# Kernel tuning notes

Measured on AMD Instinct MI355X. Metric: run time of the kernel, lower is better.

## Reference

```python
import jax, jax.numpy as jnp
import numpy as np

B, S, H, V = 4, 512, 256, 32000


def setup_inputs() -> dict:
    key = jax.random.key(0)
    ks = jax.random.split(key, 6)
    s = 0.02
    x = jax.random.randint(ks[0], (B, S), 0, V)
    emb = jax.random.normal(ks[1], (V, H), dtype=jnp.float32) * s
    W_ih = jax.random.normal(ks[2], (3 * H, H), dtype=jnp.float32) * s
    W_hh = jax.random.normal(ks[3], (3 * H, H), dtype=jnp.float32) * s
    b_ih = jnp.zeros((3 * H,), jnp.float32)
    b_hh = jnp.zeros((3 * H,), jnp.float32)
    W_out = jax.random.normal(ks[4], (V, H), dtype=jnp.float32) * s
    b_out = jnp.zeros((V,), jnp.float32)
    return dict(x=x, emb=emb, W_ih=W_ih, W_hh=W_hh, b_ih=b_ih, b_hh=b_hh,
                W_out=W_out, b_out=b_out)


def gru_sequence(embedded, W_ih, W_hh, b_ih, b_hh):
    # embedded: [B, S, H]; precompute all input projections once: [B, S, 3H]
    xp = jnp.einsum('bsh,gh->bsg', embedded, W_ih) + b_ih
    Hdim = W_hh.shape[1]
    h0 = jnp.zeros((embedded.shape[0], Hdim), embedded.dtype)

    def step(h, xt):  # xt: [B, 3H]
        hp = h @ W_hh.T + b_hh  # [B, 3H]
        xr, xz, xn = jnp.split(xt, 3, axis=-1)
        hr, hz, hn = jnp.split(hp, 3, axis=-1)
        r = jax.nn.sigmoid(xr + hr)
        z = jax.nn.sigmoid(xz + hz)
        n = jnp.tanh(xn + r * hn)
        h_new = (1.0 - z) * n + z * h
        return h_new, h_new

    _, hs = jax.lax.scan(step, h0, jnp.swapaxes(xp, 0, 1))  # [S, B, H]
    return jnp.swapaxes(hs, 0, 1)  # [B, S, H]


def reference(x, emb, W_ih, W_hh, b_ih, b_hh, W_out, b_out):
    embedded = emb[x]                                   # [B, S, H]
    rnn_out = gru_sequence(embedded, W_ih, W_hh, b_ih, b_hh)
    logits = jnp.einsum('bsh,vh->bsv', rnn_out, W_out) + b_out  # [B, S, V]
    # symbolic constraint: if prev token == 0, tokens >= 3 are invalid (t > 0)
    prev_zero = (x[:, :-1] == 0)                        # [B, S-1]
    prev_zero = jnp.pad(prev_zero, ((0, 0), (1, 0)))    # t=0 never masked
    vocab_ge3 = jnp.arange(logits.shape[-1]) >= 3       # [V]
    invalid = prev_zero[:, :, None] & vocab_ge3[None, None, :]
    return jnp.where(invalid, -jnp.inf, logits)
```

## Files before the change

### kernel.cpp

```cpp
#include <hip/hip_runtime.h>
#include <hip/hip_bf16.h>

typedef __attribute__((ext_vector_type(8))) short bf16x8;
typedef __attribute__((ext_vector_type(4))) float f32x4;
typedef __attribute__((ext_vector_type(4))) unsigned short u16x4;

#define HB 256
#define G3 768
#define SQ 512
#define NBATCH 4
#define NV 32000

__device__ __forceinline__ unsigned short f2bf(float f) {
    unsigned int u = __float_as_uint(f);
    u = u + 0x7FFFu + ((u >> 16) & 1u);
    return (unsigned short)(u >> 16);
}

__global__ void k_prep(const float* __restrict__ W_ih, const float* __restrict__ W_hh,
                       const float* __restrict__ W_out, float* __restrict__ w_ihT,
                       unsigned short* __restrict__ wfrag, unsigned short* __restrict__ woutbf,
                       int do_wout) {
    int stride = gridDim.x * blockDim.x;
    int tid = blockIdx.x * blockDim.x + threadIdx.x;
    for (int e = tid; e < G3 * HB; e += stride) {
        int k = e / G3, g = e - k * G3;
        w_ihT[e] = W_ih[g * HB + k];
    }
    for (int e = tid; e < G3 * HB; e += stride) {
        int i = e & 7, l = (e >> 3) & 63, c = (e >> 9) & 7, s = (e >> 12) & 3;
        int q = e >> 14;
        int g = q % 3, w = q / 3;
        int row = g * 256 + 64 * w + 16 * s + (l & 15);
        int kk = 32 * c + 8 * (l >> 4) + i;
        wfrag[e] = f2bf(W_hh[row * HB + kk]);
    }
    if (do_wout) {
        for (int e = tid; e < NV * HB; e += stride) woutbf[e] = f2bf(W_out[e]);
    }
}

__global__ __launch_bounds__(256) void k_embed_xp(
        const int* __restrict__ x, const float* __restrict__ emb,
        const float* __restrict__ w_ihT, const float* __restrict__ b_ih,
        const float* __restrict__ b_hh, float* __restrict__ xp) {
    __shared__ float e[8][HB];
    int tid = threadIdx.x;
    int tok0 = blockIdx.x * 8;
    {
        int s = tid >> 5, k0 = (tid & 31) * 8;
        long idx = x[tok0 + s];
        const float* src = emb + idx * (long)HB + k0;
        f32x4 a = *(const f32x4*)src, bq = *(const f32x4*)(src + 4);
        *(f32x4*)&e[s][k0] = a;
        *(f32x4*)&e[s][k0 + 4] = bq;
    }
    __syncthreads();
    #pragma unroll
    for (int it = 0; it < 3; ++it) {
        int gg = tid + it * 256;
        float acc[8] = {0.f, 0.f, 0.f, 0.f, 0.f, 0.f, 0.f, 0.f};
        for (int k = 0; k < HB; k += 4) {
            float w0 = w_ihT[(k + 0) * G3 + gg];
            float w1 = w_ihT[(k + 1) * G3 + gg];
            float w2 = w_ihT[(k + 2) * G3 + gg];
            float w3 = w_ihT[(k + 3) * G3 + gg];
            #pragma unroll
            for (int s = 0; s < 8; ++s) {
                f32x4 ev = *(const f32x4*)&e[s][k];
                acc[s] += w0 * ev.x + w1 * ev.y + w2 * ev.z + w3 * ev.w;
            }
        }
        float bias = b_ih[gg] + (gg < 512 ? b_hh[gg] : 0.f);
        #pragma unroll
        for (int s = 0; s < 8; ++s)
            xp[(size_t)(tok0 + s) * G3 + gg] = acc[s] + bias;
    }
}

__global__ __attribute__((amdgpu_waves_per_eu(1, 1))) __launch_bounds__(256)
void k_gru(const float* __restrict__ xp, const unsigned short* __restrict__ wfrag,
           const float* __restrict__ b_hh, unsigned short* __restrict__ rnn) {
    __shared__ unsigned short hbf[2][NBATCH][HB];

    int tid = threadIdx.x;
    int w = tid >> 6, l = tid & 63;
    int c15 = l & 15, hi = l >> 4;
    int b4 = c15 & 3;
    int g4 = c15 >> 2;
    int swz = (b4 & 1) << 6;

    bf16x8 Arz[2][4][8];
    bf16x8 An[4][8];
    #pragma unroll
    for (int g = 0; g < 2; ++g)
        #pragma unroll
        for (int s = 0; s < 4; ++s)
            #pragma unroll
            for (int c = 0; c < 8; ++c) {
                Arz[g][s][c] = ((const bf16x8*)wfrag)[(((w * 3 + g) * 4 + s) * 8 + c) * 64 + l];
                asm volatile("" : "+a"(Arz[g][s][c]));
            }
    #pragma unroll
    for (int s = 0; s < 4; ++s)
        #pragma unroll
        for (int c = 0; c < 8; ++c) {
            An[s][c] = ((const bf16x8*)wfrag)[(((w * 3 + 2) * 4 + c) * 8 + 0) * 64 + l];
            An[s][c] = ((const bf16x8*)wfrag)[(((w * 3 + 2) * 4 + s) * 8 + c) * 64 + l];
            asm volatile("" : "+v"(An[s][c]));
        }

    for (int k = tid; k < 2 * NBATCH * HB; k += 256) ((unsigned short*)hbf)[k] = 0;

    int iL = 64 * w + 16 * g4 + 4 * hi;
    f32x4 bnv = *(const f32x4*)&b_hh[512 + iL];
    f32x4 H = {0.f, 0.f, 0.f, 0.f};
    const f32x4 zz = {0.f, 0.f, 0.f, 0.f};

    const float* xpb = xp + (size_t)b4 * SQ * G3 + iL;
    unsigned short* rnb = rnn + (size_t)b4 * SQ * HB + iL;
    __syncthreads();

    for (int t = 0; t < SQ; ++t) {
        int cur = t & 1, nxt = cur ^ 1;
        const char* hbb = (const char*)hbf + cur * 2048 + b4 * 512;

        f32x4 xr = *(const f32x4*)(xpb);
        f32x4 xz = *(const f32x4*)(xpb + 256);
        f32x4 xn = *(const f32x4*)(xpb + 512);

        f32x4 ar[4], az[4], an[4];
        #pragma unroll
        for (int s = 0; s < 4; ++s) { ar[s] = zz; az[s] = zz; an[s] = zz; }

        #pragma unroll
        for (int c = 0; c < 8; ++c) {
            bf16x8 Bf = *(const bf16x8*)(hbb + ((64 * c + 16 * hi) ^ swz));
            #pragma unroll
            for (int s = 0; s < 4; ++s) {
                asm("v_mfma_f32_16x16x32_bf16 %0, %1, %2, %0"
                    : "+v"(ar[s]) : "a"(Arz[0][s][c]), "v"(Bf));
                asm("v_mfma_f32_16x16x32_bf16 %0, %1, %2, %0"
                    : "+v"(az[s]) : "a"(Arz[1][s][c]), "v"(Bf));
                an[s] = __builtin_amdgcn_mfma_f32_16x16x32_bf16(An[s][c], Bf, an[s], 0, 0, 0);
            }
        }
        asm volatile("s_nop 7\n\ts_nop 7"
                     : "+v"(ar[0]), "+v"(ar[1]), "+v"(ar[2]), "+v"(ar[3]),
                       "+v"(az[0]), "+v"(az[1]), "+v"(az[2]), "+v"(az[3]));

        bool s1 = (g4 & 1) != 0, s2 = (g4 & 2) != 0;
        f32x4 sAr = s2 ? (s1 ? ar[3] : ar[2]) : (s1 ? ar[1] : ar[0]);
        f32x4 sAz = s2 ? (s1 ? az[3] : az[2]) : (s1 ? az[1] : az[0]);
        f32x4 sAn = s2 ? (s1 ? an[3] : an[2]) : (s1 ? an[1] : an[0]);

        u16x4 pack;
        #pragma unroll
        for (int j = 0; j < 4; ++j) {
            float r = __builtin_amdgcn_rcpf(1.f + __expf(-(xr[j] + sAr[j])));
            float z = __builtin_amdgcn_rcpf(1.f + __expf(-(xz[j] + sAz[j])));
            float narg = xn[j] + r * (sAn[j] + bnv[j]);
            float n = 1.f - 2.f * __builtin_amdgcn_rcpf(__expf(2.f * narg) + 1.f);
            float hv = (1.f - z) * n + z * H[j];
            H[j] = hv;
            pack[j] = f2bf(hv);
        }
        *(u16x4*)((char*)hbf + nxt * 2048 + b4 * 512 + ((iL * 2) ^ swz)) = pack;
        *(u16x4*)rnb = pack;

        __syncthreads();
        xpb += G3;
        rnb += HB;
    }
}

template <int CONV>
__global__ __launch_bounds__(256) void k_logits(
        const unsigned short* __restrict__ rnn, const unsigned short* __restrict__ woutbf,
        const float* __restrict__ woutf, const float* __restrict__ b_out,
        const int* __restrict__ x, float* __restrict__ out) {
    int tid = threadIdx.x;
    int wv = tid >> 6, l = tid & 63;
    int wm = wv >> 1, wn = wv & 1;
    int c15 = l & 15, hi = l >> 4;
    int m0 = blockIdx.y * 128 + wm * 64;
    int n0 = blockIdx.x * 128 + wn * 64;

    const f32x4 zz = {0.f, 0.f, 0.f, 0.f};
    f32x4 acc[4][4];
    #pragma unroll
    for (int i = 0; i < 4; ++i)
        #pragma unroll
        for (int j = 0; j < 4; ++j) acc[i][j] = zz;

    #pragma unroll
    for (int c = 0; c < 8; ++c) {
        bf16x8 af[4], bfr[4];
        #pragma unroll
        for (int rt = 0; rt < 4; ++rt)
            af[rt] = *(const bf16x8*)(rnn + (size_t)(m0 + rt * 16 + c15) * HB + 32 * c + 8 * hi);
        #pragma unroll
        for (int ct = 0; ct < 4; ++ct) {
            if (CONV) {
                const float* s = woutf + (size_t)(n0 + ct * 16 + c15) * HB + 32 * c + 8 * hi;
                f32x4 lo = *(const f32x4*)s, hi4 = *(const f32x4*)(s + 4);
                bf16x8 bb;
                #pragma unroll
                for (int q = 0; q < 4; ++q) bb[q] = (short)f2bf(lo[q]);
                #pragma unroll
                for (int q = 0; q < 4; ++q) bb[4 + q] = (short)f2bf(hi4[q]);
                bfr[ct] = bb;
            } else {
                bfr[ct] = *(const bf16x8*)(woutbf + (size_t)(n0 + ct * 16 + c15) * HB + 32 * c + 8 * hi);
            }
        }
        #pragma unroll
        for (int rt = 0; rt < 4; ++rt)
            #pragma unroll
            for (int ct = 0; ct < 4; ++ct)
                acc[rt][ct] = __builtin_amdgcn_mfma_f32_16x16x32_bf16(af[rt], bfr[ct], acc[rt][ct], 0, 0, 0);
    }

    float bo[4];
    #pragma unroll
    for (int ct = 0; ct < 4; ++ct) bo[ct] = b_out[n0 + ct * 16 + c15];

    const float NEGINF = -__builtin_inff();
    #pragma unroll
    for (int rt = 0; rt < 4; ++rt) {
        #pragma unroll
        for (int j = 0; j < 4; ++j) {
            int m = m0 + rt * 16 + 4 * hi + j;
            int tt = m & (SQ - 1);
            bool bad = (tt > 0) && (x[m - 1] == 0);
            float* orow = out + (size_t)m * NV;
            #pragma unroll
            for (int ct = 0; ct < 4; ++ct) {
                int v = n0 + ct * 16 + c15;
                float val = acc[rt][ct][j] + bo[ct];
                if (bad && v >= 3) val = NEGINF;
                orow[v] = val;
            }
        }
    }
}

extern "C" void kernel_launch(void* const* d_in, const int* in_sizes, int n_in,
                              void* d_out, int out_size, void* d_ws, size_t ws_size,
                              hipStream_t stream) {
    const int*   x     = (const int*)d_in[0];
    const float* emb   = (const float*)d_in[1];
    const float* W_ih  = (const float*)d_in[2];
    const float* W_hh  = (const float*)d_in[3];
    const float* b_ih  = (const float*)d_in[4];
    const float* b_hh  = (const float*)d_in[5];
    const float* W_out = (const float*)d_in[6];
    const float* b_out = (const float*)d_in[7];
    float* out = (float*)d_out;

    char* ws = (char*)d_ws;
    float*          xp     = (float*)(ws);
    float*          w_ihT  = (float*)(ws + 6291456);
    unsigned short* wfrag  = (unsigned short*)(ws + 7077888);
    unsigned short* rnn    = (unsigned short*)(ws + 7471104);
    unsigned short* woutbf = (unsigned short*)(ws + 8519680);
    int use_woutbf = (ws_size >= (size_t)24903680) ? 1 : 0;

    k_prep<<<2048, 256, 0, stream>>>(W_ih, W_hh, W_out, w_ihT, wfrag, woutbf, use_woutbf);
    k_embed_xp<<<256, 256, 0, stream>>>(x, emb, w_ihT, b_ih, b_hh, xp);
    k_gru<<<1, 256, 0, stream>>>(xp, wfrag, b_hh, rnn);
    dim3 g3(NV / 128, 2048 / 128);
    if (use_woutbf)
        k_logits<0><<<g3, 256, 0, stream>>>(rnn, woutbf, nullptr, b_out, x, out);
    else
        k_logits<1><<<g3, 256, 0, stream>>>(rnn, nullptr, W_out, b_out, x, out);
}
```

Before: 910.9 us.

## Software-pipeline GRU recurrence: overlap gate activations with next gate's MFMAs

Restructures the serial GRU time-step loop so the r, z and n gate matmuls run as three separate MFMA phases. The sigmoid for r runs while the z MFMAs issue, and the sigmoid for z runs while the n MFMAs issue, so transcendental latency hides behind matrix work on the critical serial path. It also double-buffers the LDS B-fragment loads, packs h to bf16 with v_cvt_pk_bf16_f32 instead of software rounding, and replaces __syncthreads with an explicit lgkmcnt wait plus s_barrier. The volatile asm pins and manual ordering are fragile, and the hardware conversion may round slightly differently from the old software rounding.

```diff
diff --git a/kernel.cpp b/kernel.cpp
--- a/kernel.cpp
+++ b/kernel.cpp
@@ -3,7 +3,7 @@
 
 typedef __attribute__((ext_vector_type(8))) short bf16x8;
 typedef __attribute__((ext_vector_type(4))) float f32x4;
-typedef __attribute__((ext_vector_type(4))) unsigned short u16x4;
+typedef __attribute__((ext_vector_type(2))) unsigned int u32x2;
 
 #define HB 256
 #define G3 768
@@ -105,7 +105,6 @@
     for (int s = 0; s < 4; ++s)
         #pragma unroll
         for (int c = 0; c < 8; ++c) {
-            An[s][c] = ((const bf16x8*)wfrag)[(((w * 3 + 2) * 4 + c) * 8 + 0) * 64 + l];
             An[s][c] = ((const bf16x8*)wfrag)[(((w * 3 + 2) * 4 + s) * 8 + c) * 64 + l];
             asm volatile("" : "+v"(An[s][c]));
         }
@@ -116,62 +115,118 @@
     f32x4 bnv = *(const f32x4*)&b_hh[512 + iL];
     f32x4 H = {0.f, 0.f, 0.f, 0.f};
     const f32x4 zz = {0.f, 0.f, 0.f, 0.f};
+    bool s1 = (g4 & 1) != 0, s2 = (g4 & 2) != 0;
 
     const float* xpb = xp + (size_t)b4 * SQ * G3 + iL;
     unsigned short* rnb = rnn + (size_t)b4 * SQ * HB + iL;
+    const char* hbbase = (const char*)hbf + b4 * 512;
+    char* wrb = (char*)hbf + b4 * 512 + ((iL * 2) ^ swz);
     __syncthreads();
 
+#define MFA(d, g, s, c, B) \
+    asm volatile("v_mfma_f32_16x16x32_bf16 %0, %1, %2, %0" : "+v"(d) : "a"(Arz[g][s][c]), "v"(B))
+#define MFV(d, s, c, B) \
+    asm volatile("v_mfma_f32_16x16x32_bf16 %0, %1, %2, %0" : "+v"(d) : "v"(An[s][c]), "v"(B))
+#define GRP_A(q0, q1, q2, q3, g, c, B) \
+    MFA(q0, g, 0, c, B); MFA(q1, g, 1, c, B); MFA(q2, g, 2, c, B); MFA(q3, g, 3, c, B)
+#define GRP_V(q0, q1, q2, q3, c, B) \
+    MFV(q0, 0, c, B); MFV(q1, 1, c, B); MFV(q2, 2, c, B); MFV(q3, 3, c, B)
+#define PIN4(x0, x1, x2, x3) asm volatile("" : "+v"(x0), "+v"(x1), "+v"(x2), "+v"(x3))
+#define PIN1(x0) asm volatile("" : "+v"(x0))
+#define LDB(c) (*(const bf16x8*)(hbbase + cur + ((64 * (c) + 16 * hi) ^ swz)))
+#define SEL(p0, p1, p2, p3, comp) (s2 ? (s1 ? (p3).comp : (p2).comp) : (s1 ? (p1).comp : (p0).comp))
+#define SIGM(x) __builtin_amdgcn_rcpf(1.f + __expf(-(x)))
+
     for (int t = 0; t < SQ; ++t) {
-        int cur = t & 1, nxt = cur ^ 1;
-        const char* hbb = (const char*)hbf + cur * 2048 + b4 * 512;
+        int cur = (t & 1) << 11, nxt = cur ^ 2048;
 
         f32x4 xr = *(const f32x4*)(xpb);
         f32x4 xz = *(const f32x4*)(xpb + 256);
         f32x4 xn = *(const f32x4*)(xpb + 512);
 
-        f32x4 ar[4], az[4], an[4];
-        #pragma unroll
-        for (int s = 0; s < 4; ++s) { ar[s] = zz; az[s] = zz; an[s] = zz; }
-
-        #pragma unroll
-        for (int c = 0; c < 8; ++c) {
-            bf16x8 Bf = *(const bf16x8*)(hbb + ((64 * c + 16 * hi) ^ swz));
-            #pragma unroll
-            for (int s = 0; s < 4; ++s) {
-                asm("v_mfma_f32_16x16x32_bf16 %0, %1, %2, %0"
-                    : "+v"(ar[s]) : "a"(Arz[0][s][c]), "v"(Bf));
-                asm("v_mfma_f32_16x16x32_bf16 %0, %1, %2, %0"
-                    : "+v"(az[s]) : "a"(Arz[1][s][c]), "v"(Bf));
-                an[s] = __builtin_amdgcn_mfma_f32_16x16x32_bf16(An[s][c], Bf, an[s], 0, 0, 0);
-            }
-        }
-        asm volatile("s_nop 7\n\ts_nop 7"
-                     : "+v"(ar[0]), "+v"(ar[1]), "+v"(ar[2]), "+v"(ar[3]),
-                       "+v"(az[0]), "+v"(az[1]), "+v"(az[2]), "+v"(az[3]));
-
-        bool s1 = (g4 & 1) != 0, s2 = (g4 & 2) != 0;
-        f32x4 sAr = s2 ? (s1 ? ar[3] : ar[2]) : (s1 ? ar[1] : ar[0]);
-        f32x4 sAz = s2 ? (s1 ? az[3] : az[2]) : (s1 ? az[1] : az[0]);
-        f32x4 sAn = s2 ? (s1 ? an[3] : an[2]) : (s1 ? an[1] : an[0]);
-
-        u16x4 pack;
-        #pragma unroll
-        for (int j = 0; j < 4; ++j) {
-            float r = __builtin_amdgcn_rcpf(1.f + __expf(-(xr[j] + sAr[j])));
-            float z = __builtin_amdgcn_rcpf(1.f + __expf(-(xz[j] + sAz[j])));
-            float narg = xn[j] + r * (sAn[j] + bnv[j]);
-            float n = 1.f - 2.f * __builtin_amdgcn_rcpf(__expf(2.f * narg) + 1.f);
-            float hv = (1.f - z) * n + z * H[j];
-            H[j] = hv;
-            pack[j] = f2bf(hv);
-        }
-        *(u16x4*)((char*)hbf + nxt * 2048 + b4 * 512 + ((iL * 2) ^ swz)) = pack;
-        *(u16x4*)rnb = pack;
-
-        __syncthreads();
+        f32x4 a0 = zz, a1 = zz, a2 = zz, a3 = zz;
+        f32x4 z0 = zz, z1 = zz, z2 = zz, z3 = zz;
+        f32x4 n0 = zz, n1 = zz, n2 = zz, n3 = zz;
+        bf16x8 B0, B1;
+
+        B0 = LDB(0); B1 = LDB(1);
+        GRP_A(a0, a1, a2, a3, 0, 0, B0); B0 = LDB(2);
+        GRP_A(a0, a1, a2, a3, 0, 1, B1); B1 = LDB(3);
+        GRP_A(a0, a1, a2, a3, 0, 2, B0); B0 = LDB(4);
+        GRP_A(a0, a1, a2, a3, 0, 3, B1); B1 = LDB(5);
+        GRP_A(a0, a1, a2, a3, 0, 4, B0); B0 = LDB(6);
+        GRP_A(a0, a1, a2, a3, 0, 5, B1); B1 = LDB(7);
+        GRP_A(a0, a1, a2, a3, 0, 6, B0);
+        GRP_A(a0, a1, a2, a3, 0, 7, B1);
+
+        float rr0, rr1, rr2, rr3;
+        B0 = LDB(0); B1 = LDB(1);
+        GRP_A(z0, z1, z2, z3, 1, 0, B0); B0 = LDB(2);
+        PIN4(a0, a1, a2, a3);
+        GRP_A(z0, z1, z2, z3, 1, 1, B1); B1 = LDB(3);
+        rr0 = SIGM(xr.x + SEL(a0, a1, a2, a3, x));  PIN1(rr0);
+        GRP_A(z0, z1, z2, z3, 1, 2, B0); B0 = LDB(4);
+        rr1 = SIGM(xr.y + SEL(a0, a1, a2, a3, y));  PIN1(rr1);
+        GRP_A(z0, z1, z2, z3, 1, 3, B1); B1 = LDB(5);
+        rr2 = SIGM(xr.z + SEL(a0, a1, a2, a3, z));  PIN1(rr2);
+        GRP_A(z0, z1, z2, z3, 1, 4, B0); B0 = LDB(6);
+        rr3 = SIGM(xr.w + SEL(a0, a1, a2, a3, w));  PIN1(rr3);
+        GRP_A(z0, z1, z2, z3, 1, 5, B1); B1 = LDB(7);
+        GRP_A(z0, z1, z2, z3, 1, 6, B0);
+        GRP_A(z0, z1, z2, z3, 1, 7, B1);
+
+        float zg0, zg1, zg2, zg3;
+        B0 = LDB(0); B1 = LDB(1);
+        GRP_V(n0, n1, n2, n3, 0, B0); B0 = LDB(2);
+        PIN4(z0, z1, z2, z3);
+        GRP_V(n0, n1, n2, n3, 1, B1); B1 = LDB(3);
+        zg0 = SIGM(xz.x + SEL(z0, z1, z2, z3, x));  PIN1(zg0);
+        GRP_V(n0, n1, n2, n3, 2, B0); B0 = LDB(4);
+        zg1 = SIGM(xz.y + SEL(z0, z1, z2, z3, y));  PIN1(zg1);
+        GRP_V(n0, n1, n2, n3, 3, B1); B1 = LDB(5);
+        zg2 = SIGM(xz.z + SEL(z0, z1, z2, z3, z));  PIN1(zg2);
+        GRP_V(n0, n1, n2, n3, 4, B0); B0 = LDB(6);
+        zg3 = SIGM(xz.w + SEL(z0, z1, z2, z3, w));  PIN1(zg3);
+        GRP_V(n0, n1, n2, n3, 5, B1); B1 = LDB(7);
+        GRP_V(n0, n1, n2, n3, 6, B0);
+        GRP_V(n0, n1, n2, n3, 7, B1);
+
+        asm volatile("s_nop 7\n\ts_nop 7" : "+v"(n0), "+v"(n1), "+v"(n2), "+v"(n3));
+        float vn0 = SEL(n0, n1, n2, n3, x), vn1 = SEL(n0, n1, n2, n3, y);
+        float vn2 = SEL(n0, n1, n2, n3, z), vn3 = SEL(n0, n1, n2, n3, w);
+        float ng0 = 1.f - 2.f * __builtin_amdgcn_rcpf(__expf(2.f * (xn.x + rr0 * (vn0 + bnv.x))) + 1.f);
+        float ng1 = 1.f - 2.f * __builtin_amdgcn_rcpf(__expf(2.f * (xn.y + rr1 * (vn1 + bnv.y))) + 1.f);
+        float ng2 = 1.f - 2.f * __builtin_amdgcn_rcpf(__expf(2.f * (xn.z + rr2 * (vn2 + bnv.z))) + 1.f);
+        float ng3 = 1.f - 2.f * __builtin_amdgcn_rcpf(__expf(2.f * (xn.w + rr3 * (vn3 + bnv.w))) + 1.f);
+        float h0 = (1.f - zg0) * ng0 + zg0 * H.x;
+        float h1 = (1.f - zg1) * ng1 + zg1 * H.y;
+        float h2 = (1.f - zg2) * ng2 + zg2 * H.z;
+        float h3 = (1.f - zg3) * ng3 + zg3 * H.w;
+        H.x = h0; H.y = h1; H.z = h2; H.w = h3;
+
+        unsigned int p0, p1;
+        asm("v_cvt_pk_bf16_f32 %0, %1, %2" : "=v"(p0) : "v"(h0), "v"(h1));
+        asm("v_cvt_pk_bf16_f32 %0, %1, %2" : "=v"(p1) : "v"(h2), "v"(h3));
+        u32x2 pk = {p0, p1};
+        *(u32x2*)(wrb + nxt) = pk;
+        *(u32x2*)rnb = pk;
+
+        asm volatile("s_waitcnt lgkmcnt(0)" ::: "memory");
+        __builtin_amdgcn_sched_barrier(0);
+        __builtin_amdgcn_s_barrier();
+
         xpb += G3;
         rnb += HB;
     }
+#undef MFA
+#undef MFV
+#undef GRP_A
+#undef GRP_V
+#undef PIN4
+#undef PIN1
+#undef LDB
+#undef SEL
+#undef SIGM
 }
 
 template <int CONV>
@@ -206,9 +261,9 @@
                 f32x4 lo = *(const f32x4*)s, hi4 = *(const f32x4*)(s + 4);
                 bf16x8 bb;
                 #pragma unroll
-                for (int q = 0; q < 4; ++q) bb[q] = (short)f2bf(lo[q]);
+                for (int qq = 0; qq < 4; ++qq) bb[qq] = (short)f2bf(lo[qq]);
                 #pragma unroll
-                for (int q = 0; q < 4; ++q) bb[4 + q] = (short)f2bf(hi4[q]);
+                for (int qq = 0; qq < 4; ++qq) bb[4 + qq] = (short)f2bf(hi4[qq]);
                 bfr[ct] = bb;
             } else {
                 bfr[ct] = *(const bf16x8*)(woutbf + (size_t)(n0 + ct * 16 + c15) * HB + 32 * c + 8 * hi);
```

Measured after the change: 880.3 us. 1.03x faster.
